# Optimization experiments

Measured on AMD Instinct MI355X. Metric: run time of the kernel, lower is better.

Reference implementation:

```python
import jax, jax.numpy as jnp
import numpy as np

B, N, M = 1, 16384, 16384
K_NEIGH = 16
KERNEL_SIZE = 15
C_IN, C_OUT = 64, 128
RADIUS = 1.0


def setup_inputs() -> dict:
    key = jax.random.key(0)
    k1, k2, k3, k4, k5 = jax.random.split(key, 5)
    query_points = jax.random.normal(k1, (B, N, 3), dtype=jnp.float32)
    support_points = query_points  # typical KPConv: support == query
    neighbor_idx = jax.random.randint(k2, (B, N, K_NEIGH), 0, M)
    features = jax.random.normal(k3, (B, M, C_IN), dtype=jnp.float32)
    weights = jax.random.normal(k4, (KERNEL_SIZE, C_IN, C_OUT), dtype=jnp.float32) * 0.005
    # kernel points: random unit directions scaled to radius, first fixed at center
    kp = jax.random.normal(k5, (KERNEL_SIZE, 3), dtype=jnp.float32)
    kp = kp / jnp.linalg.norm(kp, axis=1, keepdims=True) * RADIUS
    kernel_points = kp.at[0].set(jnp.zeros(3, dtype=jnp.float32))
    return {
        "query_points": query_points,
        "support_points": support_points,
        "neighbor_idx": neighbor_idx,
        "features": features,
        "weights": weights,
        "kernel_points": kernel_points,
    }


def reference(query_points, support_points, neighbor_idx, features, weights, kernel_points):
    # gather neighbor features and coords: (B,N,k,C), (B,N,k,3)
    gather = jax.vmap(lambda arr, idx: arr[idx])
    neighbor_feats = gather(features, neighbor_idx)
    neighbor_coords = gather(support_points, neighbor_idx)
    # relative coords to query: (B,N,k,3)
    rel = neighbor_coords - query_points[:, :, None, :]
    # distance to each kernel point: (B,N,k,P)
    diff = rel[:, :, :, None, :] - kernel_points[None, None, None, :, :]
    dists = jnp.linalg.norm(diff, axis=-1)
    # linear influence
    infl = jnp.clip(1.0 - dists / RADIUS, 0.0)
    # weighted sum over neighbors -> (B,N,P,C) without materializing (B,N,k,P,C)
    aggregated = jnp.einsum('bnkp,bnkc->bnpc', infl, neighbor_feats)
    # per-kernel-point matmul -> (B,N,C_out)
    return jnp.einsum('bnpc,pco->bno', aggregated, weights)
```

## Files before the change

### kernel.cpp

```cpp
#include <hip/hip_runtime.h>

typedef __attribute__((ext_vector_type(8))) short bf16x8;
typedef __attribute__((ext_vector_type(4))) float f32x4;

constexpr int N_PTS = 16384;
constexpr int KN = 16;
constexpr int P  = 15;
constexpr int CI = 64;
constexpr int CO = 128;
constexpr int QB = 16;
constexpr int KTOT   = P * CI;
constexpr int KSTEPS = KTOT / 32;
constexpr int NTILES = CO / 16;
constexpr int AGG_PITCH = KTOT + 8;
constexpr int PF = 4;

static __device__ __forceinline__ unsigned short f2bf(float f) {
    unsigned u = __float_as_uint(f);
    u = (u + 0x7fffu + ((u >> 16) & 1u)) >> 16;
    return (unsigned short)u;
}

__global__ __launch_bounds__(256) void prep_w(const float* __restrict__ W,
                                              unsigned short* __restrict__ WB) {
    const int t = blockIdx.x * 256 + threadIdx.x;
    const int l  = t & 63;
    const int kb = (t >> 9) * 32 + ((l >> 4) * 8);
    const int o  = ((t >> 6) & 7) * 16 + (l & 15);
    unsigned short v[8];
    #pragma unroll
    for (int j = 0; j < 8; ++j) v[j] = f2bf(W[(size_t)(kb + j) * CO + o]);
    uint4 q;
    q.x = v[0] | ((unsigned)v[1] << 16);
    q.y = v[2] | ((unsigned)v[3] << 16);
    q.z = v[4] | ((unsigned)v[5] << 16);
    q.w = v[6] | ((unsigned)v[7] << 16);
    *(uint4*)&WB[(size_t)t * 8] = q;
}

__global__ __launch_bounds__(256) void kpconv_main(
    const float* __restrict__ query,
    const float* __restrict__ support,
    const int*   __restrict__ nidx,
    const float* __restrict__ feats,
    const unsigned short* __restrict__ WB,
    const float* __restrict__ kp,
    float* __restrict__ out)
{
    __shared__ float sKp[P][3];
    __shared__ int   sIdx[QB][KN];
    __shared__ __align__(16) float sInfl[QB][KN][16];
    __shared__ __align__(16) unsigned short sAgg[QB][AGG_PITCH];

    const int t  = threadIdx.x;
    const int n0 = blockIdx.x * QB;

    if (t < P * 3) ((float*)sKp)[t] = kp[t];
    __syncthreads();

    {
        const int pt = t >> 4, k = t & 15;
        const int n = n0 + pt;
        const int idx = nidx[n * KN + k];
        sIdx[pt][k] = idx;
        const float rx = support[idx * 3 + 0] - query[n * 3 + 0];
        const float ry = support[idx * 3 + 1] - query[n * 3 + 1];
        const float rz = support[idx * 3 + 2] - query[n * 3 + 2];
        #pragma unroll
        for (int p = 0; p < P; ++p) {
            const float dx = rx - sKp[p][0];
            const float dy = ry - sKp[p][1];
            const float dz = rz - sKp[p][2];
            sInfl[pt][k][p] = fmaxf(1.0f - sqrtf(dx*dx + dy*dy + dz*dz), 0.0f);
        }
        sInfl[pt][k][15] = 0.0f;
    }
    __syncthreads();

    {
        const int pt = t >> 4;
        const int c  = (t & 15) * 4;
        int idxv[KN];
        {
            const int4* ip = (const int4*)sIdx[pt];
            #pragma unroll
            for (int k4 = 0; k4 < 4; ++k4) {
                const int4 v = ip[k4];
                idxv[k4*4+0] = v.x; idxv[k4*4+1] = v.y;
                idxv[k4*4+2] = v.z; idxv[k4*4+3] = v.w;
            }
        }
        float acc[P][4];
        #pragma unroll
        for (int p = 0; p < P; ++p)
            #pragma unroll
            for (int j = 0; j < 4; ++j) acc[p][j] = 0.0f;

        #pragma unroll
        for (int k = 0; k < KN; ++k) {
            const float4 f = *(const float4*)&feats[(size_t)idxv[k] * CI + c];
            float iv[16];
            {
                const float4* ip = (const float4*)sInfl[pt][k];
                *(float4*)&iv[0]  = ip[0];
                *(float4*)&iv[4]  = ip[1];
                *(float4*)&iv[8]  = ip[2];
                *(float4*)&iv[12] = ip[3];
            }
            #pragma unroll
            for (int p = 0; p < P; ++p) {
                acc[p][0] = fmaf(iv[p], f.x, acc[p][0]);
                acc[p][1] = fmaf(iv[p], f.y, acc[p][1]);
                acc[p][2] = fmaf(iv[p], f.z, acc[p][2]);
                acc[p][3] = fmaf(iv[p], f.w, acc[p][3]);
            }
        }
        #pragma unroll
        for (int p = 0; p < P; ++p) {
            uint2 w;
            w.x = f2bf(acc[p][0]) | ((unsigned)f2bf(acc[p][1]) << 16);
            w.y = f2bf(acc[p][2]) | ((unsigned)f2bf(acc[p][3]) << 16);
            *(uint2*)&sAgg[pt][p * CI + c] = w;
        }
    }
    __syncthreads();

    {
        const int w = t >> 6, l = t & 63;
        const int row = l & 15;
        const int kq  = (l >> 4) * 8;
        f32x4 c0 = {0.f, 0.f, 0.f, 0.f};
        f32x4 c1 = {0.f, 0.f, 0.f, 0.f};
        const unsigned short* aggRow = &sAgg[row][kq];
        const unsigned short* wb0 = &WB[(size_t)(2 * w * 64 + l) * 8];
        bf16x8 pb0[PF], pb1[PF];
        #pragma unroll
        for (int s = 0; s < PF; ++s) {
            pb0[s] = *(const bf16x8*)&wb0[(size_t)s * 4096];
            pb1[s] = *(const bf16x8*)&wb0[(size_t)s * 4096 + 512];
        }
        #pragma unroll
        for (int s = 0; s < KSTEPS; ++s) {
            const bf16x8 a = *(const bf16x8*)&aggRow[s * 32];
            c0 = __builtin_amdgcn_mfma_f32_16x16x32_bf16(a, pb0[s & (PF - 1)], c0, 0, 0, 0);
            c1 = __builtin_amdgcn_mfma_f32_16x16x32_bf16(a, pb1[s & (PF - 1)], c1, 0, 0, 0);
            if (s + PF < KSTEPS) {
                pb0[s & (PF - 1)] = *(const bf16x8*)&wb0[(size_t)(s + PF) * 4096];
                pb1[s & (PF - 1)] = *(const bf16x8*)&wb0[(size_t)(s + PF) * 4096 + 512];
            }
        }
        const int rbase = (l >> 4) * 4;
        const int o0 = 2 * w * 16 + (l & 15);
        #pragma unroll
        for (int r = 0; r < 4; ++r) {
            const int pt = rbase + r;
            out[(size_t)(n0 + pt) * CO + o0]      = c0[r];
            out[(size_t)(n0 + pt) * CO + o0 + 16] = c1[r];
        }
    }
}

extern "C" void kernel_launch(void* const* d_in, const int* in_sizes, int n_in,
                              void* d_out, int out_size, void* d_ws, size_t ws_size,
                              hipStream_t stream) {
    const float* query   = (const float*)d_in[0];
    const float* support = (const float*)d_in[1];
    const int*   nidx    = (const int*)d_in[2];
    const float* feats   = (const float*)d_in[3];
    const float* W       = (const float*)d_in[4];
    const float* kp      = (const float*)d_in[5];
    float* out = (float*)d_out;
    unsigned short* WB = (unsigned short*)d_ws;

    hipLaunchKernelGGL(prep_w, dim3(60), dim3(256), 0, stream, W, WB);
    hipLaunchKernelGGL(kpconv_main, dim3(N_PTS / QB), dim3(256), 0, stream,
                       query, support, nidx, feats, WB, kp, out);
}
```

Before: 90.67 us.

## Skip zero-influence neighbors, double query tile, share weight fragments across rows

Each neighbor's influence is checked during influence computation, and only neighbors with nonzero influence are kept in a compact per-query list. The aggregation loop then iterates only over that list. The block grows to 32 queries and 512 threads, so each wave reuses a single weight fragment for two MFMA row tiles. Influences are stored as bf16 and indices as 16-bit values, which assumes M fits in 16 bits and adds rounding.

```diff
diff --git a/kernel.cpp b/kernel.cpp
--- a/kernel.cpp
+++ b/kernel.cpp
@@ -8,11 +8,10 @@
 constexpr int P  = 15;
 constexpr int CI = 64;
 constexpr int CO = 128;
-constexpr int QB = 16;
+constexpr int QB = 32;
 constexpr int KTOT   = P * CI;
 constexpr int KSTEPS = KTOT / 32;
-constexpr int NTILES = CO / 16;
-constexpr int AGG_PITCH = KTOT + 8;
+constexpr int APITCH = KTOT + 8;
 constexpr int PF = 4;
 
 static __device__ __forceinline__ unsigned short f2bf(float f) {
@@ -20,6 +19,8 @@
     u = (u + 0x7fffu + ((u >> 16) & 1u)) >> 16;
     return (unsigned short)u;
 }
+#define BFLO(u) __uint_as_float((unsigned)(u) << 16)
+#define BFHI(u) __uint_as_float((unsigned)(u) & 0xFFFF0000u)
 
 __global__ __launch_bounds__(256) void prep_w(const float* __restrict__ W,
                                               unsigned short* __restrict__ WB) {
@@ -38,7 +39,7 @@
     *(uint4*)&WB[(size_t)t * 8] = q;
 }
 
-__global__ __launch_bounds__(256) void kpconv_main(
+__global__ __launch_bounds__(512, 4) void kpconv_main(
     const float* __restrict__ query,
     const float* __restrict__ support,
     const int*   __restrict__ nidx,
@@ -48,114 +49,116 @@
     float* __restrict__ out)
 {
     __shared__ float sKp[P][3];
-    __shared__ int   sIdx[QB][KN];
-    __shared__ __align__(16) float sInfl[QB][KN][16];
-    __shared__ __align__(16) unsigned short sAgg[QB][AGG_PITCH];
+    __shared__ unsigned short sIdxS[QB][KN];
+    __shared__ int sCnt[QB];
+    __shared__ unsigned char sKlist[QB][KN];
+    __shared__ __align__(16) unsigned short sInflB[QB][KN][16];
+    __shared__ __align__(16) unsigned short sAgg[QB][APITCH];
 
     const int t  = threadIdx.x;
     const int n0 = blockIdx.x * QB;
+    const int w  = t >> 6, l = t & 63;
 
     if (t < P * 3) ((float*)sKp)[t] = kp[t];
+    if (t < QB) sCnt[t] = 0;
     __syncthreads();
 
     {
         const int pt = t >> 4, k = t & 15;
         const int n = n0 + pt;
         const int idx = nidx[n * KN + k];
-        sIdx[pt][k] = idx;
+        sIdxS[pt][k] = (unsigned short)idx;
         const float rx = support[idx * 3 + 0] - query[n * 3 + 0];
         const float ry = support[idx * 3 + 1] - query[n * 3 + 1];
         const float rz = support[idx * 3 + 2] - query[n * 3 + 2];
+        unsigned short h[16];
+        float mx = 0.0f;
         #pragma unroll
         for (int p = 0; p < P; ++p) {
             const float dx = rx - sKp[p][0];
             const float dy = ry - sKp[p][1];
             const float dz = rz - sKp[p][2];
-            sInfl[pt][k][p] = fmaxf(1.0f - sqrtf(dx*dx + dy*dy + dz*dz), 0.0f);
+            const float infl = fmaxf(1.0f - sqrtf(dx*dx + dy*dy + dz*dz), 0.0f);
+            mx = fmaxf(mx, infl);
+            h[p] = f2bf(infl);
         }
-        sInfl[pt][k][15] = 0.0f;
+        h[15] = 0;
+        uint4 u0, u1;
+        u0.x = h[0] | ((unsigned)h[1] << 16);   u0.y = h[2] | ((unsigned)h[3] << 16);
+        u0.z = h[4] | ((unsigned)h[5] << 16);   u0.w = h[6] | ((unsigned)h[7] << 16);
+        u1.x = h[8] | ((unsigned)h[9] << 16);   u1.y = h[10] | ((unsigned)h[11] << 16);
+        u1.z = h[12] | ((unsigned)h[13] << 16); u1.w = h[14];
+        *(uint4*)&sInflB[pt][k][0] = u0;
+        *(uint4*)&sInflB[pt][k][8] = u1;
+        if (mx > 0.0f) {
+            const int slot = atomicAdd(&sCnt[pt], 1);
+            sKlist[pt][slot] = (unsigned char)k;
+        }
     }
     __syncthreads();
 
     {
         const int pt = t >> 4;
         const int c  = (t & 15) * 4;
-        int idxv[KN];
-        {
-            const int4* ip = (const int4*)sIdx[pt];
-            #pragma unroll
-            for (int k4 = 0; k4 < 4; ++k4) {
-                const int4 v = ip[k4];
-                idxv[k4*4+0] = v.x; idxv[k4*4+1] = v.y;
-                idxv[k4*4+2] = v.z; idxv[k4*4+3] = v.w;
-            }
+        const int nk = sCnt[pt];
+        f32x4 A0={0,0,0,0},A1={0,0,0,0},A2={0,0,0,0},A3={0,0,0,0},A4={0,0,0,0};
+        f32x4 A5={0,0,0,0},A6={0,0,0,0},A7={0,0,0,0},A8={0,0,0,0},A9={0,0,0,0};
+        f32x4 A10={0,0,0,0},A11={0,0,0,0},A12={0,0,0,0},A13={0,0,0,0},A14={0,0,0,0};
+        for (int i = 0; i < nk; ++i) {
+            const int k   = sKlist[pt][i];
+            const int idx = sIdxS[pt][k];
+            const f32x4 fv = *(const f32x4*)&feats[(size_t)idx * CI + c];
+            const uint4 u0 = *(const uint4*)&sInflB[pt][k][0];
+            const uint4 u1 = *(const uint4*)&sInflB[pt][k][8];
+            A0  += BFLO(u0.x) * fv;  A1  += BFHI(u0.x) * fv;
+            A2  += BFLO(u0.y) * fv;  A3  += BFHI(u0.y) * fv;
+            A4  += BFLO(u0.z) * fv;  A5  += BFHI(u0.z) * fv;
+            A6  += BFLO(u0.w) * fv;  A7  += BFHI(u0.w) * fv;
+            A8  += BFLO(u1.x) * fv;  A9  += BFHI(u1.x) * fv;
+            A10 += BFLO(u1.y) * fv;  A11 += BFHI(u1.y) * fv;
+            A12 += BFLO(u1.z) * fv;  A13 += BFHI(u1.z) * fv;
+            A14 += BFLO(u1.w) * fv;
         }
-        float acc[P][4];
-        #pragma unroll
-        for (int p = 0; p < P; ++p)
-            #pragma unroll
-            for (int j = 0; j < 4; ++j) acc[p][j] = 0.0f;
-
-        #pragma unroll
-        for (int k = 0; k < KN; ++k) {
-            const float4 f = *(const float4*)&feats[(size_t)idxv[k] * CI + c];
-            float iv[16];
-            {
-                const float4* ip = (const float4*)sInfl[pt][k];
-                *(float4*)&iv[0]  = ip[0];
-                *(float4*)&iv[4]  = ip[1];
-                *(float4*)&iv[8]  = ip[2];
-                *(float4*)&iv[12] = ip[3];
-            }
-            #pragma unroll
-            for (int p = 0; p < P; ++p) {
-                acc[p][0] = fmaf(iv[p], f.x, acc[p][0]);
-                acc[p][1] = fmaf(iv[p], f.y, acc[p][1]);
-                acc[p][2] = fmaf(iv[p], f.z, acc[p][2]);
-                acc[p][3] = fmaf(iv[p], f.w, acc[p][3]);
-            }
-        }
-        #pragma unroll
-        for (int p = 0; p < P; ++p) {
-            uint2 w;
-            w.x = f2bf(acc[p][0]) | ((unsigned)f2bf(acc[p][1]) << 16);
-            w.y = f2bf(acc[p][2]) | ((unsigned)f2bf(acc[p][3]) << 16);
-            *(uint2*)&sAgg[pt][p * CI + c] = w;
-        }
+        #define STORE_P(p, Ap)                                                  \
+            do {                                                                \
+                uint2 wv;                                                       \
+                wv.x = f2bf(Ap.x) | ((unsigned)f2bf(Ap.y) << 16);               \
+                wv.y = f2bf(Ap.z) | ((unsigned)f2bf(Ap.w) << 16);               \
+                *(uint2*)&sAgg[pt][(p) * CI + c] = wv;                          \
+            } while (0)
+        STORE_P(0, A0);  STORE_P(1, A1);  STORE_P(2, A2);  STORE_P(3, A3);
+        STORE_P(4, A4);  STORE_P(5, A5);  STORE_P(6, A6);  STORE_P(7, A7);
+        STORE_P(8, A8);  STORE_P(9, A9);  STORE_P(10, A10); STORE_P(11, A11);
+        STORE_P(12, A12); STORE_P(13, A13); STORE_P(14, A14);
+        #undef STORE_P
     }
     __syncthreads();
 
     {
-        const int w = t >> 6, l = t & 63;
-        const int row = l & 15;
-        const int kq  = (l >> 4) * 8;
         f32x4 c0 = {0.f, 0.f, 0.f, 0.f};
         f32x4 c1 = {0.f, 0.f, 0.f, 0.f};
-        const unsigned short* aggRow = &sAgg[row][kq];
-        const unsigned short* wb0 = &WB[(size_t)(2 * w * 64 + l) * 8];
-        bf16x8 pb0[PF], pb1[PF];
+        const int kq = (l >> 4) * 8;
+        const unsigned short* a0 = &sAgg[l & 15][kq];
+        const unsigned short* a1 = &sAgg[16 + (l & 15)][kq];
+        const unsigned short* wb = &WB[(size_t)(w * 64 + l) * 8];
+        bf16x8 pb[PF];
         #pragma unroll
-        for (int s = 0; s < PF; ++s) {
-            pb0[s] = *(const bf16x8*)&wb0[(size_t)s * 4096];
-            pb1[s] = *(const bf16x8*)&wb0[(size_t)s * 4096 + 512];
-        }
+        for (int s = 0; s < PF; ++s) pb[s] = *(const bf16x8*)&wb[(size_t)s * 4096];
         #pragma unroll
         for (int s = 0; s < KSTEPS; ++s) {
-            const bf16x8 a = *(const bf16x8*)&aggRow[s * 32];
-            c0 = __builtin_amdgcn_mfma_f32_16x16x32_bf16(a, pb0[s & (PF - 1)], c0, 0, 0, 0);
-            c1 = __builtin_amdgcn_mfma_f32_16x16x32_bf16(a, pb1[s & (PF - 1)], c1, 0, 0, 0);
-            if (s + PF < KSTEPS) {
-                pb0[s & (PF - 1)] = *(const bf16x8*)&wb0[(size_t)(s + PF) * 4096];
-                pb1[s & (PF - 1)] = *(const bf16x8*)&wb0[(size_t)(s + PF) * 4096 + 512];
-            }
+            const bf16x8 av0 = *(const bf16x8*)&a0[s * 32];
+            const bf16x8 av1 = *(const bf16x8*)&a1[s * 32];
+            const bf16x8 bv = pb[s & (PF - 1)];
+            c0 = __builtin_amdgcn_mfma_f32_16x16x32_bf16(av0, bv, c0, 0, 0, 0);
+            c1 = __builtin_amdgcn_mfma_f32_16x16x32_bf16(av1, bv, c1, 0, 0, 0);
+            if (s + PF < KSTEPS) pb[s & (PF - 1)] = *(const bf16x8*)&wb[(size_t)(s + PF) * 4096];
         }
-        const int rbase = (l >> 4) * 4;
-        const int o0 = 2 * w * 16 + (l & 15);
+        const int o0 = w * 16 + (l & 15);
+        const int r0 = n0 + (l >> 4) * 4;
         #pragma unroll
         for (int r = 0; r < 4; ++r) {
-            const int pt = rbase + r;
-            out[(size_t)(n0 + pt) * CO + o0]      = c0[r];
-            out[(size_t)(n0 + pt) * CO + o0 + 16] = c1[r];
+            out[(size_t)(r0 + r) * CO + o0]      = c0[r];
+            out[(size_t)(r0 + 16 + r) * CO + o0] = c1[r];
         }
     }
 }
@@ -173,6 +176,6 @@
     unsigned short* WB = (unsigned short*)d_ws;
 
     hipLaunchKernelGGL(prep_w, dim3(60), dim3(256), 0, stream, W, WB);
-    hipLaunchKernelGGL(kpconv_main, dim3(N_PTS / QB), dim3(256), 0, stream,
+    hipLaunchKernelGGL(kpconv_main, dim3(N_PTS / QB), dim3(512), 0, stream,
                        query, support, nidx, feats, WB, kp, out);
 }
```

New measurement: 86.24 us. 1.05x faster.
